# Performance work log

Hardware: AMD Instinct MI355X
Metric: run time of the kernel (lower is better)

The kernel has to match this reference:

```python
import jax, jax.numpy as jnp
import numpy as np

B, T, H_IMG, HID, ACT = 128, 100, 72, 512, 2


def _conv(x, w, b, stride, pad):
    y = jax.lax.conv_general_dilated(
        x, w, (stride, stride), [(pad, pad), (pad, pad)],
        dimension_numbers=('NCHW', 'OIHW', 'NCHW'))
    return y + b[None, :, None, None]


def _encode(images, cw1, cb1, cw2, cb2, cw3, cb3, fw1, fb1, fw2, fb2, fw3, fb3):
    relu = jax.nn.relu
    x = relu(_conv(images, cw1, cb1, 3, 2))   # [B,64,24,24]
    x = relu(_conv(x, cw2, cb2, 3, 2))        # [B,64,9,9]
    x = relu(_conv(x, cw3, cb3, 3, 2))        # [B,64,4,4]
    x = x.reshape(x.shape[0], -1)             # [B,1024]
    x = relu(x @ fw1.T + fb1)
    x = relu(x @ fw2.T + fb2)
    return x @ fw3.T + fb3                    # [B,512]


def _gru(actions, h0, w_ih, w_hh, b_ih, b_hh):
    # precompute input projections for all steps: [T,B,3H]
    gi = jnp.einsum('btd,gd->tbg', actions, w_ih) + b_ih

    def step(h, gi_t):
        gh = h @ w_hh.T + b_hh
        i_r, i_i, i_n = jnp.split(gi_t, 3, axis=-1)
        h_r, h_i, h_n = jnp.split(gh, 3, axis=-1)
        r = jax.nn.sigmoid(i_r + h_r)
        z = jax.nn.sigmoid(i_i + h_i)
        n = jnp.tanh(i_n + r * h_n)
        hy = n + z * (h - n)
        return hy, hy

    hT, outs = jax.lax.scan(step, h0, gi)
    return jnp.transpose(outs, (1, 0, 2)), hT  # batch_first output


def setup_inputs() -> dict:
    key = jax.random.key(0)
    ks = jax.random.split(key, 16)
    s = 0.05
    return {
        'images': jax.random.normal(ks[0], (B, 3, H_IMG, H_IMG), jnp.float32),
        'actions': jax.random.normal(ks[1], (B, T, ACT), jnp.float32),
        'cw1': jax.random.normal(ks[2], (64, 3, 5, 5), jnp.float32) * s,
        'cb1': jax.random.normal(ks[3], (64,), jnp.float32) * s,
        'cw2': jax.random.normal(ks[4], (64, 64, 3, 3), jnp.float32) * s,
        'cb2': jax.random.normal(ks[5], (64,), jnp.float32) * s,
        'cw3': jax.random.normal(ks[6], (64, 64, 3, 3), jnp.float32) * s,
        'cb3': jax.random.normal(ks[7], (64,), jnp.float32) * s,
        'fw1': jax.random.normal(ks[8], (1024, 1024), jnp.float32) * 0.02,
        'fb1': jax.random.normal(ks[9], (1024,), jnp.float32) * 0.02,
        'fw2': jax.random.normal(ks[10], (512, 1024), jnp.float32) * 0.02,
        'fb2': jax.random.normal(ks[11], (512,), jnp.float32) * 0.02,
        'fw3': jax.random.normal(ks[12], (512, 512), jnp.float32) * 0.02,
        'fb3': jax.random.normal(ks[13], (512,), jnp.float32) * 0.02,
        'w_ih': jax.random.normal(ks[14], (3 * HID, ACT), jnp.float32) * 0.05,
        'w_hh': jax.random.normal(ks[15], (3 * HID, HID), jnp.float32) * 0.04,
        'b_ih': jnp.zeros((3 * HID,), jnp.float32),
        'b_hh': jnp.zeros((3 * HID,), jnp.float32),
    }


def reference(images, actions, cw1, cb1, cw2, cb2, cw3, cb3,
              fw1, fb1, fw2, fb2, fw3, fb3, w_ih, w_hh, b_ih, b_hh):
    # Encode the start image to a 512-d representation (BigBasicConv),
    # then integrate the action sequence with the hand-rolled GRU,
    # initial hidden state = start representation.
    h0 = _encode(images, cw1, cb1, cw2, cb2, cw3, cb3,
                 fw1, fb1, fw2, fb2, fw3, fb3)
    output, hT = _gru(actions, h0, w_ih, w_hh, b_ih, b_hh)
    return output, hT
```

## Files before the change

kernel.cpp:

```cpp
#include <hip/hip_runtime.h>
#include <cstdint>

#define BB   128
#define TT   100
#define HID  512

typedef __attribute__((ext_vector_type(4))) float f32x4;
typedef __attribute__((ext_vector_type(2))) float f32x2;
typedef __attribute__((ext_vector_type(8))) short short8;
typedef __attribute__((ext_vector_type(4))) short short4_t;

__device__ __forceinline__ short f2bf(float x) {
  unsigned u = __float_as_uint(x);
  unsigned r = (u + 0x7fffu + ((u >> 16) & 1u)) >> 16;
  return (short)r;
}
__device__ __forceinline__ float bf2f(short s) {
  return __uint_as_float(((unsigned)(unsigned short)s) << 16);
}

__global__ __launch_bounds__(256) void wsplit_k(const float* __restrict__ w,
                                                unsigned short* __restrict__ hi,
                                                unsigned short* __restrict__ lo,
                                                int nq) {
  int i = blockIdx.x * 256 + threadIdx.x;
  const int stride = gridDim.x * 256;
  for (; i < nq; i += stride) {
    f32x4 v = *(const f32x4*)(w + 4 * (long)i);
    short4_t h, l;
    #pragma unroll
    for (int c = 0; c < 4; c++) {
      short hh = f2bf(v[c]); h[c] = hh; l[c] = f2bf(v[c] - bf2f(hh));
    }
    *(short4_t*)(hi + 4 * (long)i) = h;
    *(short4_t*)(lo + 4 * (long)i) = l;
  }
}


__global__ __launch_bounds__(192) void conv1_k(const float* __restrict__ in,
                                               const float* __restrict__ w,
                                               const float* __restrict__ bias,
                                               float* __restrict__ out) {
  const int b = blockIdx.x / 24, oy = blockIdx.x % 24;
  __shared__ __attribute__((aligned(16))) float in_s[3][5][76];
  __shared__ __attribute__((aligned(16))) float ws[64][76];
  const int tid = threadIdx.x;
  for (int i = tid; i < 3 * 5 * 76; i += 192) {
    int ic = i / 380, rem = i % 380, r = rem / 76, p = rem % 76;
    int iy = oy * 3 + r - 2, ix = p - 2;
    in_s[ic][r][p] = (iy >= 0 && iy < 72 && ix >= 0 && ix < 72)
                       ? in[((long)(b * 3 + ic) * 72 + iy) * 72 + ix] : 0.f;
  }
  for (int i = tid; i < 64 * 75; i += 192) ws[i / 75][i % 75] = w[i];
  __syncthreads();

  const int ox2 = tid % 12;
  const int og = tid / 12;
  float strip[15][8];
  #pragma unroll
  for (int ic = 0; ic < 3; ic++)
    #pragma unroll
    for (int ky = 0; ky < 5; ky++) {
      const float* bp = &in_s[ic][ky][6 * ox2];
      #pragma unroll
      for (int h = 0; h < 4; h++) {
        f32x2 u = *(const f32x2*)(bp + 2 * h);
        strip[ic * 5 + ky][2 * h] = u[0];
        strip[ic * 5 + ky][2 * h + 1] = u[1];
      }
    }

  #pragma unroll
  for (int j = 0; j < 4; j++) {
    const int oc = og + 16 * j;
    float s0 = bias[oc], s1 = bias[oc];
    const float* wrow = ws[oc];
    #pragma unroll
    for (int k4 = 0; k4 < 18; k4++) {
      f32x4 wq = *(const f32x4*)(wrow + 4 * k4);
      #pragma unroll
      for (int q = 0; q < 4; q++) {
        const int k = 4 * k4 + q, i5 = k / 5, kx = k % 5;
        s0 += strip[i5][kx] * wq[q];
        s1 += strip[i5][kx + 3] * wq[q];
      }
    }
    s0 += strip[14][2] * wrow[72]; s1 += strip[14][5] * wrow[72];
    s0 += strip[14][3] * wrow[73]; s1 += strip[14][6] * wrow[73];
    s0 += strip[14][4] * wrow[74]; s1 += strip[14][7] * wrow[74];
    long o = ((long)(b * 64 + oc) * 24 + oy) * 24 + 2 * ox2;
    out[o] = fmaxf(s0, 0.f);
    out[o + 1] = fmaxf(s1, 0.f);
  }
}

template <int IC, int IH, int IW, int OC, int OH, int OW>
__global__ void convs3(const float* __restrict__ in, const float* __restrict__ w,
                       const float* __restrict__ bias, float* __restrict__ out) {
  const int b = blockIdx.x / OH, oy = blockIdx.x % OH;
  constexpr int PW = 3 * OW;
  constexpr int NT = (OC / 2) * OW;
  __shared__ __attribute__((aligned(16))) float in_s[8][3][PW];
  __shared__ __attribute__((aligned(16))) float w_s[OC][100];
  const int tid = threadIdx.x;
  const int oc = tid / OW, ox = tid % OW;
  float s0 = bias[oc], s1 = bias[oc + OC / 2];
  for (int cc = 0; cc < IC; cc += 8) {
    __syncthreads();
    for (int i = tid; i < 8 * 3 * PW; i += NT) {
      int ic = i / (3 * PW), r = (i / PW) % 3, p = i % PW;
      int iy = oy * 3 - 2 + r, ix = p - 2;
      in_s[ic][r][p] = (iy >= 0 && iy < IH && ix >= 0 && ix < IW)
                         ? in[((long)(b * IC + cc + ic) * IH + iy) * IW + ix] : 0.f;
    }
    for (int i = tid; i < OC * 8 * 9; i += NT) {
      int o = i / 72, r = i % 72;
      w_s[o][(r / 9) * 12 + (r % 9)] = w[(long)(o * IC + cc + r / 9) * 9 + r % 9];
    }
    __syncthreads();
    #pragma unroll
    for (int ic = 0; ic < 8; ic++) {
      const float* wr0 = &w_s[oc][ic * 12];
      const float* wr1 = &w_s[oc + OC / 2][ic * 12];
      f32x4 wa = *(const f32x4*)wr0, wb = *(const f32x4*)(wr0 + 4);
      f32x4 va = *(const f32x4*)wr1, vb = *(const f32x4*)(wr1 + 4);
      float wA[9] = {wa[0], wa[1], wa[2], wa[3], wb[0], wb[1], wb[2], wb[3], wr0[8]};
      float wB[9] = {va[0], va[1], va[2], va[3], vb[0], vb[1], vb[2], vb[3], wr1[8]};
      #pragma unroll
      for (int ky = 0; ky < 3; ky++)
        #pragma unroll
        for (int kx = 0; kx < 3; kx++) {
          float iv = in_s[ic][ky][ox * 3 + kx];
          s0 += iv * wA[ky * 3 + kx];
          s1 += iv * wB[ky * 3 + kx];
        }
    }
  }
  out[((long)(b * OC + oc) * OH + oy) * OW + ox] = fmaxf(s0, 0.f);
  out[((long)(b * OC + oc + OC / 2) * OH + oy) * OW + ox] = fmaxf(s1, 0.f);
}

template <int K, int N, bool RELU>
__global__ __launch_bounds__(128) void fc_mfma(const float* __restrict__ A,
                                               const unsigned short* __restrict__ wh,
                                               const unsigned short* __restrict__ wl,
                                               const float* __restrict__ bias,
                                               float* __restrict__ C) {
  const int nb = N / 32;
  const int rb = (blockIdx.x / nb) * 16, cb = (blockIdx.x % nb) * 32;
  __shared__ __attribute__((aligned(16))) short A_hi[16][K + 8];
  __shared__ __attribute__((aligned(16))) short A_lo[16][K + 8];
  const int tid = threadIdx.x;
  const int wv = tid >> 6, lane = tid & 63, n16 = lane & 15, quad = lane >> 4;

  for (int i = tid; i < 16 * (K / 4); i += 128) {
    int row = i / (K / 4), q = i % (K / 4);
    f32x4 v = *(const f32x4*)(A + (long)(rb + row) * K + 4 * q);
    short4_t sh, sl;
    #pragma unroll
    for (int c = 0; c < 4; c++) {
      short hh = f2bf(v[c]); sh[c] = hh; sl[c] = f2bf(v[c] - bf2f(hh));
    }
    *(short4_t*)&A_hi[row][4 * q] = sh;
    *(short4_t*)&A_lo[row][4 * q] = sl;
  }
  __syncthreads();

  const int col = cb + wv * 16 + n16;
  f32x4 a0 = {0.f, 0.f, 0.f, 0.f}, a1 = a0, a2 = a0;
  constexpr int NP = K / 512;
  #pragma unroll 1
  for (int p = 0; p < NP; p++) {
    short8 fh[16], fl[16];
    const unsigned short* wb0 = wh + (long)col * K + p * 512 + quad * 8;
    const unsigned short* wb1 = wl + (long)col * K + p * 512 + quad * 8;
    #pragma unroll
    for (int ks = 0; ks < 16; ks++) {
      fh[ks] = *(const short8*)(wb0 + ks * 32);
      fl[ks] = *(const short8*)(wb1 + ks * 32);
    }
    #pragma unroll
    for (int ks = 0; ks < 16; ks++) {
      short8 ah = *(const short8*)&A_hi[n16][p * 512 + ks * 32 + quad * 8];
      short8 al = *(const short8*)&A_lo[n16][p * 512 + ks * 32 + quad * 8];
      a0 = __builtin_amdgcn_mfma_f32_16x16x32_bf16(ah, fh[ks], a0, 0, 0, 0);
      a1 = __builtin_amdgcn_mfma_f32_16x16x32_bf16(al, fh[ks], a1, 0, 0, 0);
      a2 = __builtin_amdgcn_mfma_f32_16x16x32_bf16(ah, fl[ks], a2, 0, 0, 0);
    }
  }
  const float bv = bias[col];
  #pragma unroll
  for (int r = 0; r < 4; r++) {
    float v = a0[r] + a1[r] + a2[r] + bv;
    if (RELU) v = fmaxf(v, 0.f);
    C[(long)(rb + quad * 4 + r) * N + col] = v;
  }
}

__global__ __launch_bounds__(192, 1) void gru_k(
    const float* __restrict__ actions, const float* __restrict__ w_ih,
    const float* __restrict__ w_hh, const float* __restrict__ b_ih,
    const float* __restrict__ b_hh, const float* __restrict__ h0,
    float* __restrict__ out, float* __restrict__ hT, unsigned* __restrict__ bar) {
  const int bg = blockIdx.x >> 5;
  const int hg = blockIdx.x & 31;
  const int tid = threadIdx.x;
  const int wv = tid >> 6;
  const int lane = tid & 63;
  const int n16 = lane & 15;
  const int quad = lane >> 4;

  __shared__ short h_hi[16][520];
  __shared__ short h_lo[16][520];
  __shared__ float act_s[16][2 * TT];
  __shared__ float gh_s[3][16][17];
  __shared__ float bih_s[48], bhh_s[48], wih0_s[48], wih1_s[48];

  short8 whi[16], wlo[16];
  {
    const int grow = wv * HID + hg * 16 + n16;
    const float* wr = w_hh + (long)grow * HID + quad * 8;
    #pragma unroll
    for (int ks = 0; ks < 16; ks++) {
      f32x4 v0 = *(const f32x4*)(wr + ks * 32);
      f32x4 v1 = *(const f32x4*)(wr + ks * 32 + 4);
      short8 hi, lo;
      #pragma unroll
      for (int j = 0; j < 4; j++) {
        short h1 = f2bf(v0[j]); hi[j] = h1;     lo[j] = f2bf(v0[j] - bf2f(h1));
        short h2 = f2bf(v1[j]); hi[j + 4] = h2; lo[j + 4] = f2bf(v1[j] - bf2f(h2));
      }
      whi[ks] = hi; wlo[ks] = lo;
    }
  }
  for (int i = tid; i < 48; i += 192) {
    int row = (i >> 4) * HID + hg * 16 + (i & 15);
    bih_s[i] = b_ih[row];
    bhh_s[i] = b_hh[row];
    wih0_s[i] = w_ih[row * 2];
    wih1_s[i] = w_ih[row * 2 + 1];
  }
  for (int i = tid; i < 16 * 2 * TT; i += 192) {
    int m = i / (2 * TT), r = i % (2 * TT);
    act_s[m][r] = actions[(long)(bg * 16 + m) * (2 * TT) + r];
  }
  for (int i = tid; i < 2048; i += 192) {
    int m = i >> 7, k4 = (i & 127) << 2;
    f32x4 v = *(const f32x4*)(h0 + (long)(bg * 16 + m) * HID + k4);
    short4_t sh, sl;
    #pragma unroll
    for (int c2 = 0; c2 < 4; c2++) {
      short hh = f2bf(v[c2]); sh[c2] = hh; sl[c2] = f2bf(v[c2] - bf2f(hh));
    }
    *(short4_t*)&h_hi[m][k4] = sh;
    *(short4_t*)&h_lo[m][k4] = sl;
  }
  __syncthreads();

  unsigned* my_bar = bar + bg * 32;

  #pragma unroll 1
  for (int t = 0; t < TT; t++) {
    f32x4 a0 = {0.f, 0.f, 0.f, 0.f}, a1 = a0, a2 = a0;
    #pragma unroll
    for (int ks = 0; ks < 16; ks++) {
      short8 ah = *(const short8*)&h_hi[n16][ks * 32 + quad * 8];
      short8 al = *(const short8*)&h_lo[n16][ks * 32 + quad * 8];
      a0 = __builtin_amdgcn_mfma_f32_16x16x32_bf16(ah, whi[ks], a0, 0, 0, 0);
      a1 = __builtin_amdgcn_mfma_f32_16x16x32_bf16(al, whi[ks], a1, 0, 0, 0);
      a2 = __builtin_amdgcn_mfma_f32_16x16x32_bf16(ah, wlo[ks], a2, 0, 0, 0);
    }
    #pragma unroll
    for (int r = 0; r < 4; r++)
      gh_s[wv][quad * 4 + r][n16] = a0[r] + a1[r] + a2[r];
    __syncthreads();

    if (tid < 128) {
      const int m = tid >> 3;
      const int n0 = (tid & 7) << 1;
      const float x0 = act_s[m][2 * t], x1 = act_s[m][2 * t + 1];
      float hy[2];
      #pragma unroll
      for (int q = 0; q < 2; q++) {
        int n = n0 + q;
        float hr = gh_s[0][m][n] + bhh_s[n];
        float hz = gh_s[1][m][n] + bhh_s[16 + n];
        float hn = gh_s[2][m][n] + bhh_s[32 + n];
        float ir = x0 * wih0_s[n]      + x1 * wih1_s[n]      + bih_s[n];
        float iz = x0 * wih0_s[16 + n] + x1 * wih1_s[16 + n] + bih_s[16 + n];
        float in_ = x0 * wih0_s[32 + n] + x1 * wih1_s[32 + n] + bih_s[32 + n];
        float rg = 1.f / (1.f + __expf(-(ir + hr)));
        float zg = 1.f / (1.f + __expf(-(iz + hz)));
        float nx = in_ + rg * hn;
        float ng = 1.f - 2.f / (__expf(2.f * nx) + 1.f);
        float hprev = bf2f(h_hi[m][hg * 16 + n]) + bf2f(h_lo[m][hg * 16 + n]);
        hy[q] = ng + zg * (hprev - ng);
      }
      unsigned long long pack = (unsigned long long)__float_as_uint(hy[0]) |
                                ((unsigned long long)__float_as_uint(hy[1]) << 32);
      __hip_atomic_store(
          (unsigned long long*)&out[((long)(bg * 16 + m) * TT + t) * HID + hg * 16 + n0],
          pack, __ATOMIC_RELAXED, __HIP_MEMORY_SCOPE_AGENT);
      if (t == TT - 1)
        *(unsigned long long*)&hT[(long)(bg * 16 + m) * HID + hg * 16 + n0] = pack;
    }
    __syncthreads();

    if (t < TT - 1) {
      if (tid == 0) {
        const unsigned target = 32u * (unsigned)(t + 1);
        unsigned prev = __hip_atomic_fetch_add(my_bar, 1u, __ATOMIC_RELAXED,
                                               __HIP_MEMORY_SCOPE_AGENT);
        if (prev + 1u < target) {
          while (__hip_atomic_load(my_bar, __ATOMIC_RELAXED,
                                   __HIP_MEMORY_SCOPE_AGENT) < target)
            __builtin_amdgcn_s_sleep(1);
        }
      }
      __syncthreads();
      unsigned long long vbuf[22];
      #pragma unroll
      for (int u = 0; u < 21; u++) {
        int i = tid + u * 192;
        int m = i >> 8, j = (i & 255) << 1;
        vbuf[u] = __hip_atomic_load(
            (const unsigned long long*)(out + ((long)(bg * 16 + m) * TT + t) * HID + j),
            __ATOMIC_RELAXED, __HIP_MEMORY_SCOPE_AGENT);
      }
      if (tid < 64) {
        int i = 4032 + tid;
        int m = i >> 8, j = (i & 255) << 1;
        vbuf[21] = __hip_atomic_load(
            (const unsigned long long*)(out + ((long)(bg * 16 + m) * TT + t) * HID + j),
            __ATOMIC_RELAXED, __HIP_MEMORY_SCOPE_AGENT);
      }
      #pragma unroll
      for (int u = 0; u < 21; u++) {
        int i = tid + u * 192;
        int m = i >> 8, j = (i & 255) << 1;
        unsigned long long v = vbuf[u];
        float f0 = __uint_as_float((unsigned)v);
        float f1 = __uint_as_float((unsigned)(v >> 32));
        short s0 = f2bf(f0);
        h_hi[m][j] = s0; h_lo[m][j] = f2bf(f0 - bf2f(s0));
        short s1 = f2bf(f1);
        h_hi[m][j + 1] = s1; h_lo[m][j + 1] = f2bf(f1 - bf2f(s1));
      }
      if (tid < 64) {
        int i = 4032 + tid;
        int m = i >> 8, j = (i & 255) << 1;
        unsigned long long v = vbuf[21];
        float f0 = __uint_as_float((unsigned)v);
        float f1 = __uint_as_float((unsigned)(v >> 32));
        short s0 = f2bf(f0);
        h_hi[m][j] = s0; h_lo[m][j] = f2bf(f0 - bf2f(s0));
        short s1 = f2bf(f1);
        h_hi[m][j + 1] = s1; h_lo[m][j + 1] = f2bf(f1 - bf2f(s1));
      }
      __syncthreads();
    }
  }
}

extern "C" void kernel_launch(void* const* d_in, const int* in_sizes, int n_in,
                              void* d_out, int out_size, void* d_ws, size_t ws_size,
                              hipStream_t stream) {
  const float* images  = (const float*)d_in[0];
  const float* actions = (const float*)d_in[1];
  const float* cw1 = (const float*)d_in[2];
  const float* cb1 = (const float*)d_in[3];
  const float* cw2 = (const float*)d_in[4];
  const float* cb2 = (const float*)d_in[5];
  const float* cw3 = (const float*)d_in[6];
  const float* cb3 = (const float*)d_in[7];
  const float* fw1 = (const float*)d_in[8];
  const float* fb1 = (const float*)d_in[9];
  const float* fw2 = (const float*)d_in[10];
  const float* fb2 = (const float*)d_in[11];
  const float* fw3 = (const float*)d_in[12];
  const float* fb3 = (const float*)d_in[13];
  const float* w_ih = (const float*)d_in[14];
  const float* w_hh = (const float*)d_in[15];
  const float* b_ih = (const float*)d_in[16];
  const float* b_hh = (const float*)d_in[17];

  char* ws = (char*)d_ws;
  unsigned* bar = (unsigned*)ws;
  float* a1 = (float*)(ws + 1024);
  float* a2 = a1 + (long)128 * 64 * 576;
  float* a3 = a2 + (long)128 * 64 * 81;
  float* f1 = a3 + (long)128 * 1024;
  float* f2 = f1 + (long)128 * 1024;
  float* h0 = f2 + (long)128 * 512;
  unsigned short* wfh1 = (unsigned short*)(h0 + 65536);
  unsigned short* wfl1 = wfh1 + (long)1048576;
  unsigned short* wfh2 = wfl1 + (long)1048576;
  unsigned short* wfl2 = wfh2 + (long)524288;
  unsigned short* wfh3 = wfl2 + (long)524288;
  unsigned short* wfl3 = wfh3 + (long)262144;

  float* out = (float*)d_out;
  float* hT  = out + (long)BB * TT * HID;

  hipMemsetAsync(bar, 0, 1024, stream);
  wsplit_k<<<256, 256, 0, stream>>>(fw1, wfh1, wfl1, 262144);
  wsplit_k<<<128, 256, 0, stream>>>(fw2, wfh2, wfl2, 131072);
  wsplit_k<<<64, 256, 0, stream>>>(fw3, wfh3, wfl3, 65536);
  conv1_k<<<128 * 24, 192, 0, stream>>>(images, cw1, cb1, a1);
  convs3<64, 24, 24, 64, 9, 9><<<128 * 9, 288, 0, stream>>>(a1, cw2, cb2, a2);
  convs3<64, 9, 9, 64, 4, 4><<<128 * 4, 128, 0, stream>>>(a2, cw3, cb3, a3);
  fc_mfma<1024, 1024, true><<<256, 128, 0, stream>>>(a3, wfh1, wfl1, fb1, f1);
  fc_mfma<1024, 512, true><<<128, 128, 0, stream>>>(f1, wfh2, wfl2, fb2, f2);
  fc_mfma<512, 512, false><<<128, 128, 0, stream>>>(f2, wfh3, wfl3, fb3, h0);
  gru_k<<<256, 192, 0, stream>>>(actions, w_ih, w_hh, b_ih, b_hh, h0, out, hT, bar);
}
```

Before: 645.1 us.

## Fuse conv2, conv3, FC layers and GRU into one persistent kernel

Merges conv2, conv3, the three FC layers and the GRU into a single persistent 256-block kernel, with grid-wide atomic barriers between phases in place of separate launches. The three weight-split kernels also become one launch, and the GRU carries its previous hidden state in registers. The goal is to remove launch overhead and inter-kernel gaps. In exchange, the conv phases are re-tiled onto a fixed grid of 256 blocks with 192 threads, which may lower per-phase efficiency, and the spin barriers depend on all 256 blocks being co-resident.

```diff
diff --git a/kernel.cpp b/kernel.cpp
--- a/kernel.cpp
+++ b/kernel.cpp
@@ -9,6 +9,7 @@
 typedef __attribute__((ext_vector_type(2))) float f32x2;
 typedef __attribute__((ext_vector_type(8))) short short8;
 typedef __attribute__((ext_vector_type(4))) short short4_t;
+typedef unsigned long long ull;
 
 __device__ __forceinline__ short f2bf(float x) {
   unsigned u = __float_as_uint(x);
@@ -18,25 +19,45 @@
 __device__ __forceinline__ float bf2f(short s) {
   return __uint_as_float(((unsigned)(unsigned short)s) << 16);
 }
-
-__global__ __launch_bounds__(256) void wsplit_k(const float* __restrict__ w,
-                                                unsigned short* __restrict__ hi,
-                                                unsigned short* __restrict__ lo,
-                                                int nq) {
+__device__ __forceinline__ ull aload8(const void* p) {
+  return __hip_atomic_load((const ull*)p, __ATOMIC_RELAXED, __HIP_MEMORY_SCOPE_AGENT);
+}
+__device__ __forceinline__ void astore8(void* p, ull v) {
+  __hip_atomic_store((ull*)p, v, __ATOMIC_RELAXED, __HIP_MEMORY_SCOPE_AGENT);
+}
+__device__ __forceinline__ float aloadf(const float* p) {
+  unsigned v = __hip_atomic_load((const unsigned*)p, __ATOMIC_RELAXED,
+                                 __HIP_MEMORY_SCOPE_AGENT);
+  return __uint_as_float(v);
+}
+__device__ __forceinline__ void astoref(float* p, float x) {
+  __hip_atomic_store((unsigned*)p, __float_as_uint(x), __ATOMIC_RELAXED,
+                     __HIP_MEMORY_SCOPE_AGENT);
+}
+
+__global__ __launch_bounds__(256) void wsplit_all(
+    const float* __restrict__ w1, const float* __restrict__ w2,
+    const float* __restrict__ w3, unsigned short* __restrict__ h1,
+    unsigned short* __restrict__ l1, unsigned short* __restrict__ h2,
+    unsigned short* __restrict__ l2, unsigned short* __restrict__ h3,
+    unsigned short* __restrict__ l3) {
   int i = blockIdx.x * 256 + threadIdx.x;
   const int stride = gridDim.x * 256;
-  for (; i < nq; i += stride) {
-    f32x4 v = *(const f32x4*)(w + 4 * (long)i);
+  for (; i < 458752; i += stride) {
+    const float* src; unsigned short *ph, *pl; int j;
+    if (i < 262144)      { src = w1; ph = h1; pl = l1; j = i; }
+    else if (i < 393216) { src = w2; ph = h2; pl = l2; j = i - 262144; }
+    else                 { src = w3; ph = h3; pl = l3; j = i - 393216; }
+    f32x4 v = *(const f32x4*)(src + 4 * (long)j);
     short4_t h, l;
     #pragma unroll
     for (int c = 0; c < 4; c++) {
       short hh = f2bf(v[c]); h[c] = hh; l[c] = f2bf(v[c] - bf2f(hh));
     }
-    *(short4_t*)(hi + 4 * (long)i) = h;
-    *(short4_t*)(lo + 4 * (long)i) = l;
-  }
-}
-
+    *(short4_t*)(ph + 4 * (long)j) = h;
+    *(short4_t*)(pl + 4 * (long)j) = l;
+  }
+}
 
 __global__ __launch_bounds__(192) void conv1_k(const float* __restrict__ in,
                                                const float* __restrict__ w,
@@ -95,270 +116,402 @@
   }
 }
 
-template <int IC, int IH, int IW, int OC, int OH, int OW>
-__global__ void convs3(const float* __restrict__ in, const float* __restrict__ w,
-                       const float* __restrict__ bias, float* __restrict__ out) {
-  const int b = blockIdx.x / OH, oy = blockIdx.x % OH;
-  constexpr int PW = 3 * OW;
-  constexpr int NT = (OC / 2) * OW;
-  __shared__ __attribute__((aligned(16))) float in_s[8][3][PW];
-  __shared__ __attribute__((aligned(16))) float w_s[OC][100];
-  const int tid = threadIdx.x;
-  const int oc = tid / OW, ox = tid % OW;
-  float s0 = bias[oc], s1 = bias[oc + OC / 2];
-  for (int cc = 0; cc < IC; cc += 8) {
-    __syncthreads();
-    for (int i = tid; i < 8 * 3 * PW; i += NT) {
-      int ic = i / (3 * PW), r = (i / PW) % 3, p = i % PW;
-      int iy = oy * 3 - 2 + r, ix = p - 2;
-      in_s[ic][r][p] = (iy >= 0 && iy < IH && ix >= 0 && ix < IW)
-                         ? in[((long)(b * IC + cc + ic) * IH + iy) * IW + ix] : 0.f;
-    }
-    for (int i = tid; i < OC * 8 * 9; i += NT) {
-      int o = i / 72, r = i % 72;
-      w_s[o][(r / 9) * 12 + (r % 9)] = w[(long)(o * IC + cc + r / 9) * 9 + r % 9];
-    }
-    __syncthreads();
-    #pragma unroll
-    for (int ic = 0; ic < 8; ic++) {
-      const float* wr0 = &w_s[oc][ic * 12];
-      const float* wr1 = &w_s[oc + OC / 2][ic * 12];
-      f32x4 wa = *(const f32x4*)wr0, wb = *(const f32x4*)(wr0 + 4);
-      f32x4 va = *(const f32x4*)wr1, vb = *(const f32x4*)(wr1 + 4);
-      float wA[9] = {wa[0], wa[1], wa[2], wa[3], wb[0], wb[1], wb[2], wb[3], wr0[8]};
-      float wB[9] = {va[0], va[1], va[2], va[3], vb[0], vb[1], vb[2], vb[3], wr1[8]};
-      #pragma unroll
-      for (int ky = 0; ky < 3; ky++)
-        #pragma unroll
-        for (int kx = 0; kx < 3; kx++) {
-          float iv = in_s[ic][ky][ox * 3 + kx];
-          s0 += iv * wA[ky * 3 + kx];
-          s1 += iv * wB[ky * 3 + kx];
-        }
-    }
-  }
-  out[((long)(b * OC + oc) * OH + oy) * OW + ox] = fmaxf(s0, 0.f);
-  out[((long)(b * OC + oc + OC / 2) * OH + oy) * OW + ox] = fmaxf(s1, 0.f);
+
+__device__ __forceinline__ void gbarrier(unsigned* c) {
+  __syncthreads();
+  if (threadIdx.x == 0) {
+    __hip_atomic_fetch_add(c, 1u, __ATOMIC_RELAXED, __HIP_MEMORY_SCOPE_AGENT);
+    while (__hip_atomic_load(c, __ATOMIC_RELAXED, __HIP_MEMORY_SCOPE_AGENT) < 256u)
+      __builtin_amdgcn_s_sleep(2);
+  }
+  __syncthreads();
 }
 
 template <int K, int N, bool RELU>
-__global__ __launch_bounds__(128) void fc_mfma(const float* __restrict__ A,
-                                               const unsigned short* __restrict__ wh,
-                                               const unsigned short* __restrict__ wl,
-                                               const float* __restrict__ bias,
-                                               float* __restrict__ C) {
+__device__ __forceinline__ void fc_phase(int bid, int tid, const float* A,
+    const unsigned short* wh, const unsigned short* wl, const float* bias,
+    float* C, char* smem) {
   const int nb = N / 32;
-  const int rb = (blockIdx.x / nb) * 16, cb = (blockIdx.x % nb) * 32;
-  __shared__ __attribute__((aligned(16))) short A_hi[16][K + 8];
-  __shared__ __attribute__((aligned(16))) short A_lo[16][K + 8];
-  const int tid = threadIdx.x;
+  if (bid >= (BB / 16) * nb) return;
+  short (*A_hi)[520] = (short(*)[520])smem;
+  short (*A_lo)[520] = (short(*)[520])(smem + 16 * 520 * 2);
+  const int rb = (bid / nb) * 16, cb = (bid % nb) * 32;
   const int wv = tid >> 6, lane = tid & 63, n16 = lane & 15, quad = lane >> 4;
-
-  for (int i = tid; i < 16 * (K / 4); i += 128) {
-    int row = i / (K / 4), q = i % (K / 4);
-    f32x4 v = *(const f32x4*)(A + (long)(rb + row) * K + 4 * q);
-    short4_t sh, sl;
-    #pragma unroll
-    for (int c = 0; c < 4; c++) {
-      short hh = f2bf(v[c]); sh[c] = hh; sl[c] = f2bf(v[c] - bf2f(hh));
-    }
-    *(short4_t*)&A_hi[row][4 * q] = sh;
-    *(short4_t*)&A_lo[row][4 * q] = sl;
-  }
-  __syncthreads();
-
   const int col = cb + wv * 16 + n16;
   f32x4 a0 = {0.f, 0.f, 0.f, 0.f}, a1 = a0, a2 = a0;
-  constexpr int NP = K / 512;
   #pragma unroll 1
-  for (int p = 0; p < NP; p++) {
-    short8 fh[16], fl[16];
-    const unsigned short* wb0 = wh + (long)col * K + p * 512 + quad * 8;
-    const unsigned short* wb1 = wl + (long)col * K + p * 512 + quad * 8;
+  for (int p = 0; p < K / 512; p++) {
+    if (p) __syncthreads();
+    for (int i = tid; i < 2048; i += 192) {
+      int row = i >> 7, q = i & 127;
+      const float* src = A + (long)(rb + row) * K + p * 512 + 4 * q;
+      union { ull u[2]; float f[4]; } v;
+      v.u[0] = aload8(src); v.u[1] = aload8(src + 2);
+      short4_t sh, sl;
+      #pragma unroll
+      for (int c = 0; c < 4; c++) {
+        short hh = f2bf(v.f[c]); sh[c] = hh; sl[c] = f2bf(v.f[c] - bf2f(hh));
+      }
+      *(short4_t*)&A_hi[row][4 * q] = sh;
+      *(short4_t*)&A_lo[row][4 * q] = sl;
+    }
+    __syncthreads();
+    if (tid < 128) {
+      const unsigned short* wb0 = wh + (long)col * K + p * 512 + quad * 8;
+      const unsigned short* wb1 = wl + (long)col * K + p * 512 + quad * 8;
+      short8 fh[16], fl[16];
+      #pragma unroll
+      for (int ks = 0; ks < 16; ks++) {
+        fh[ks] = *(const short8*)(wb0 + ks * 32);
+        fl[ks] = *(const short8*)(wb1 + ks * 32);
+      }
+      #pragma unroll
+      for (int ks = 0; ks < 16; ks++) {
+        short8 ah = *(const short8*)&A_hi[n16][ks * 32 + quad * 8];
+        short8 al = *(const short8*)&A_lo[n16][ks * 32 + quad * 8];
+        a0 = __builtin_amdgcn_mfma_f32_16x16x32_bf16(ah, fh[ks], a0, 0, 0, 0);
+        a1 = __builtin_amdgcn_mfma_f32_16x16x32_bf16(al, fh[ks], a1, 0, 0, 0);
+        a2 = __builtin_amdgcn_mfma_f32_16x16x32_bf16(ah, fl[ks], a2, 0, 0, 0);
+      }
+    }
+  }
+  if (tid < 128) {
+    const float bv = bias[col];
     #pragma unroll
-    for (int ks = 0; ks < 16; ks++) {
-      fh[ks] = *(const short8*)(wb0 + ks * 32);
-      fl[ks] = *(const short8*)(wb1 + ks * 32);
-    }
-    #pragma unroll
-    for (int ks = 0; ks < 16; ks++) {
-      short8 ah = *(const short8*)&A_hi[n16][p * 512 + ks * 32 + quad * 8];
-      short8 al = *(const short8*)&A_lo[n16][p * 512 + ks * 32 + quad * 8];
-      a0 = __builtin_amdgcn_mfma_f32_16x16x32_bf16(ah, fh[ks], a0, 0, 0, 0);
-      a1 = __builtin_amdgcn_mfma_f32_16x16x32_bf16(al, fh[ks], a1, 0, 0, 0);
-      a2 = __builtin_amdgcn_mfma_f32_16x16x32_bf16(ah, fl[ks], a2, 0, 0, 0);
-    }
-  }
-  const float bv = bias[col];
-  #pragma unroll
-  for (int r = 0; r < 4; r++) {
-    float v = a0[r] + a1[r] + a2[r] + bv;
-    if (RELU) v = fmaxf(v, 0.f);
-    C[(long)(rb + quad * 4 + r) * N + col] = v;
-  }
-}
-
-__global__ __launch_bounds__(192, 1) void gru_k(
+    for (int r = 0; r < 4; r++) {
+      float v = a0[r] + a1[r] + a2[r] + bv;
+      if (RELU) v = fmaxf(v, 0.f);
+      astoref(&C[(long)(rb + quad * 4 + r) * N + col], v);
+    }
+  }
+}
+
+__global__ __launch_bounds__(192, 1) void mega_k(
+    const float* __restrict__ a1, const float* __restrict__ cw2,
+    const float* __restrict__ cb2, const float* __restrict__ cw3,
+    const float* __restrict__ cb3,
+    const unsigned short* __restrict__ wfh1, const unsigned short* __restrict__ wfl1,
+    const float* __restrict__ fb1,
+    const unsigned short* __restrict__ wfh2, const unsigned short* __restrict__ wfl2,
+    const float* __restrict__ fb2,
+    const unsigned short* __restrict__ wfh3, const unsigned short* __restrict__ wfl3,
+    const float* __restrict__ fb3,
     const float* __restrict__ actions, const float* __restrict__ w_ih,
     const float* __restrict__ w_hh, const float* __restrict__ b_ih,
-    const float* __restrict__ b_hh, const float* __restrict__ h0,
-    float* __restrict__ out, float* __restrict__ hT, unsigned* __restrict__ bar) {
-  const int bg = blockIdx.x >> 5;
-  const int hg = blockIdx.x & 31;
+    const float* __restrict__ b_hh,
+    float* __restrict__ a2, float* __restrict__ a3, float* __restrict__ f1,
+    float* __restrict__ f2, float* __restrict__ h0,
+    float* __restrict__ out, float* __restrict__ hT,
+    unsigned* __restrict__ bar, unsigned* __restrict__ gctr) {
+  __shared__ __attribute__((aligned(16))) char smem[50176];
+  const int bid = blockIdx.x;
   const int tid = threadIdx.x;
-  const int wv = tid >> 6;
-  const int lane = tid & 63;
-  const int n16 = lane & 15;
-  const int quad = lane >> 4;
-
-  __shared__ short h_hi[16][520];
-  __shared__ short h_lo[16][520];
-  __shared__ float act_s[16][2 * TT];
-  __shared__ float gh_s[3][16][17];
-  __shared__ float bih_s[48], bhh_s[48], wih0_s[48], wih1_s[48];
-
-  short8 whi[16], wlo[16];
+
   {
-    const int grow = wv * HID + hg * 16 + n16;
-    const float* wr = w_hh + (long)grow * HID + quad * 8;
-    #pragma unroll
-    for (int ks = 0; ks < 16; ks++) {
-      f32x4 v0 = *(const f32x4*)(wr + ks * 32);
-      f32x4 v1 = *(const f32x4*)(wr + ks * 32 + 4);
-      short8 hi, lo;
-      #pragma unroll
-      for (int j = 0; j < 4; j++) {
-        short h1 = f2bf(v0[j]); hi[j] = h1;     lo[j] = f2bf(v0[j] - bf2f(h1));
-        short h2 = f2bf(v1[j]); hi[j + 4] = h2; lo[j + 4] = f2bf(v1[j] - bf2f(h2));
-      }
-      whi[ks] = hi; wlo[ks] = lo;
-    }
-  }
-  for (int i = tid; i < 48; i += 192) {
-    int row = (i >> 4) * HID + hg * 16 + (i & 15);
-    bih_s[i] = b_ih[row];
-    bhh_s[i] = b_hh[row];
-    wih0_s[i] = w_ih[row * 2];
-    wih1_s[i] = w_ih[row * 2 + 1];
-  }
-  for (int i = tid; i < 16 * 2 * TT; i += 192) {
-    int m = i / (2 * TT), r = i % (2 * TT);
-    act_s[m][r] = actions[(long)(bg * 16 + m) * (2 * TT) + r];
-  }
-  for (int i = tid; i < 2048; i += 192) {
-    int m = i >> 7, k4 = (i & 127) << 2;
-    f32x4 v = *(const f32x4*)(h0 + (long)(bg * 16 + m) * HID + k4);
-    short4_t sh, sl;
-    #pragma unroll
-    for (int c2 = 0; c2 < 4; c2++) {
-      short hh = f2bf(v[c2]); sh[c2] = hh; sl[c2] = f2bf(v[c2] - bf2f(hh));
-    }
-    *(short4_t*)&h_hi[m][k4] = sh;
-    *(short4_t*)&h_lo[m][k4] = sl;
-  }
-  __syncthreads();
-
-  unsigned* my_bar = bar + bg * 32;
-
-  #pragma unroll 1
-  for (int t = 0; t < TT; t++) {
-    f32x4 a0 = {0.f, 0.f, 0.f, 0.f}, a1 = a0, a2 = a0;
-    #pragma unroll
-    for (int ks = 0; ks < 16; ks++) {
-      short8 ah = *(const short8*)&h_hi[n16][ks * 32 + quad * 8];
-      short8 al = *(const short8*)&h_lo[n16][ks * 32 + quad * 8];
-      a0 = __builtin_amdgcn_mfma_f32_16x16x32_bf16(ah, whi[ks], a0, 0, 0, 0);
-      a1 = __builtin_amdgcn_mfma_f32_16x16x32_bf16(al, whi[ks], a1, 0, 0, 0);
-      a2 = __builtin_amdgcn_mfma_f32_16x16x32_bf16(ah, wlo[ks], a2, 0, 0, 0);
-    }
-    #pragma unroll
-    for (int r = 0; r < 4; r++)
-      gh_s[wv][quad * 4 + r][n16] = a0[r] + a1[r] + a2[r];
+    float (*w_s)[100] = (float(*)[100])smem;
+    float* in2 = (float*)(smem + 25600);
+    const int q = tid / 9, ox = tid % 9;
+    float acc[5][4];
+    if (tid < 144) {
+      #pragma unroll
+      for (int t5 = 0; t5 < 5; t5++)
+        #pragma unroll
+        for (int j = 0; j < 4; j++) acc[t5][j] = cb2[q + 16 * j];
+    }
+    for (int cc = 0; cc < 64; cc += 8) {
+      __syncthreads();
+      for (int i = tid; i < 4608; i += 192) {
+        int o = i / 72, r = i % 72;
+        w_s[o][(r / 9) * 12 + (r % 9)] = cw2[(long)(o * 64 + cc + r / 9) * 9 + r % 9];
+      }
+      for (int i = tid; i < 3240; i += 192) {
+        int t5 = i / 648, r = i % 648;
+        int tile = bid + t5 * 256;
+        if (tile < 1152) {
+          int b = tile / 9, oy = tile % 9;
+          int ic = r / 81, rr = (r / 27) % 3, p = r % 27;
+          int iy = oy * 3 - 2 + rr, ix = p - 2;
+          in2[t5 * 648 + ic * 81 + rr * 27 + p] =
+              (iy >= 0 && iy < 24 && ix >= 0 && ix < 24)
+                ? a1[((long)(b * 64 + cc + ic) * 24 + iy) * 24 + ix] : 0.f;
+        }
+      }
+      __syncthreads();
+      if (tid < 144) {
+        #pragma unroll
+        for (int ic = 0; ic < 8; ic++) {
+          float wq[4][9];
+          #pragma unroll
+          for (int j = 0; j < 4; j++) {
+            const float* wr = &w_s[q + 16 * j][ic * 12];
+            f32x4 wa = *(const f32x4*)wr, wb = *(const f32x4*)(wr + 4);
+            wq[j][0] = wa[0]; wq[j][1] = wa[1]; wq[j][2] = wa[2]; wq[j][3] = wa[3];
+            wq[j][4] = wb[0]; wq[j][5] = wb[1]; wq[j][6] = wb[2]; wq[j][7] = wb[3];
+            wq[j][8] = wr[8];
+          }
+          #pragma unroll
+          for (int t5 = 0; t5 < 5; t5++) {
+            if (bid + t5 * 256 < 1152) {
+              #pragma unroll
+              for (int ky = 0; ky < 3; ky++)
+                #pragma unroll
+                for (int kx = 0; kx < 3; kx++) {
+                  float iv = in2[t5 * 648 + ic * 81 + ky * 27 + ox * 3 + kx];
+                  #pragma unroll
+                  for (int j = 0; j < 4; j++) acc[t5][j] += iv * wq[j][ky * 3 + kx];
+                }
+            }
+          }
+        }
+      }
+    }
+    if (tid < 144) {
+      #pragma unroll
+      for (int t5 = 0; t5 < 5; t5++) {
+        int tile = bid + t5 * 256;
+        if (tile < 1152) {
+          int b = tile / 9, oy = tile % 9;
+          #pragma unroll
+          for (int j = 0; j < 4; j++)
+            astoref(&a2[((long)(b * 64 + q + 16 * j) * 9 + oy) * 9 + ox],
+                    fmaxf(acc[t5][j], 0.f));
+        }
+      }
+    }
+  }
+  gbarrier(gctr + 0);
+
+  {
+    float (*w_s)[100] = (float(*)[100])smem;
+    float* in3 = (float*)(smem + 25600);
+    const int oc = tid >> 2, ox = tid & 3;
+    float acc[2][2];
+    if (tid < 128) {
+      acc[0][0] = acc[1][0] = cb3[oc];
+      acc[0][1] = acc[1][1] = cb3[oc + 32];
+    }
+    for (int cc = 0; cc < 64; cc += 8) {
+      __syncthreads();
+      for (int i = tid; i < 4608; i += 192) {
+        int o = i / 72, r = i % 72;
+        w_s[o][(r / 9) * 12 + (r % 9)] = cw3[(long)(o * 64 + cc + r / 9) * 9 + r % 9];
+      }
+      for (int i = tid; i < 576; i += 192) {
+        int t2 = i / 288, r = i % 288;
+        int tile = bid + t2 * 256;
+        int b = tile / 4, oy = tile % 4;
+        int ic = r / 36, rr = (r / 12) % 3, p = r % 12;
+        int iy = oy * 3 - 2 + rr, ix = p - 2;
+        in3[t2 * 288 + ic * 36 + rr * 12 + p] =
+            (iy >= 0 && iy < 9 && ix >= 0 && ix < 9)
+              ? aloadf(&a2[((long)(b * 64 + cc + ic) * 9 + iy) * 9 + ix]) : 0.f;
+      }
+      __syncthreads();
+      if (tid < 128) {
+        #pragma unroll
+        for (int ic = 0; ic < 8; ic++) {
+          const float* wr0 = &w_s[oc][ic * 12];
+          const float* wr1 = &w_s[oc + 32][ic * 12];
+          f32x4 wa = *(const f32x4*)wr0, wb = *(const f32x4*)(wr0 + 4);
+          f32x4 va = *(const f32x4*)wr1, vb = *(const f32x4*)(wr1 + 4);
+          float wA[9] = {wa[0], wa[1], wa[2], wa[3], wb[0], wb[1], wb[2], wb[3], wr0[8]};
+          float wB[9] = {va[0], va[1], va[2], va[3], vb[0], vb[1], vb[2], vb[3], wr1[8]};
+          #pragma unroll
+          for (int t2 = 0; t2 < 2; t2++)
+            #pragma unroll
+            for (int ky = 0; ky < 3; ky++)
+              #pragma unroll
+              for (int kx = 0; kx < 3; kx++) {
+                float iv = in3[t2 * 288 + ic * 36 + ky * 12 + ox * 3 + kx];
+                acc[t2][0] += iv * wA[ky * 3 + kx];
+                acc[t2][1] += iv * wB[ky * 3 + kx];
+              }
+        }
+      }
+    }
+    if (tid < 128) {
+      #pragma unroll
+      for (int t2 = 0; t2 < 2; t2++) {
+        int tile = bid + t2 * 256;
+        int b = tile / 4, oy = tile % 4;
+        astoref(&a3[((long)(b * 64 + oc) * 4 + oy) * 4 + ox], fmaxf(acc[t2][0], 0.f));
+        astoref(&a3[((long)(b * 64 + oc + 32) * 4 + oy) * 4 + ox], fmaxf(acc[t2][1], 0.f));
+      }
+    }
+  }
+  gbarrier(gctr + 1);
+
+  fc_phase<1024, 1024, true>(bid, tid, a3, wfh1, wfl1, fb1, f1, smem);
+  gbarrier(gctr + 2);
+  fc_phase<1024, 512, true>(bid, tid, f1, wfh2, wfl2, fb2, f2, smem);
+  gbarrier(gctr + 3);
+  fc_phase<512, 512, false>(bid, tid, f2, wfh3, wfl3, fb3, h0, smem);
+  gbarrier(gctr + 4);
+
+  {
+    short (*h_hi)[520] = (short(*)[520])smem;
+    short (*h_lo)[520] = (short(*)[520])(smem + 16640);
+    float (*act_s)[200] = (float(*)[200])(smem + 33280);
+    float (*gh_s)[16][17] = (float(*)[16][17])(smem + 46080);
+    float* bih_s = (float*)(smem + 49344);
+    float* bhh_s = bih_s + 48;
+    float* wih0_s = bhh_s + 48;
+    float* wih1_s = wih0_s + 48;
+
+    const int bg = bid >> 5;
+    const int hg = bid & 31;
+    const int wv = tid >> 6;
+    const int lane = tid & 63;
+    const int n16 = lane & 15;
+    const int quad = lane >> 4;
+
+    short8 whi[16], wlo[16];
+    {
+      const int grow = wv * HID + hg * 16 + n16;
+      const float* wr = w_hh + (long)grow * HID + quad * 8;
+      #pragma unroll
+      for (int ks = 0; ks < 16; ks++) {
+        f32x4 v0 = *(const f32x4*)(wr + ks * 32);
+        f32x4 v1 = *(const f32x4*)(wr + ks * 32 + 4);
+        short8 hi, lo;
+        #pragma unroll
+        for (int j = 0; j < 4; j++) {
+          short h1 = f2bf(v0[j]); hi[j] = h1;     lo[j] = f2bf(v0[j] - bf2f(h1));
+          short h2 = f2bf(v1[j]); hi[j + 4] = h2; lo[j + 4] = f2bf(v1[j] - bf2f(h2));
+        }
+        whi[ks] = hi; wlo[ks] = lo;
+      }
+    }
+    for (int i = tid; i < 48; i += 192) {
+      int row = (i >> 4) * HID + hg * 16 + (i & 15);
+      bih_s[i] = b_ih[row];
+      bhh_s[i] = b_hh[row];
+      wih0_s[i] = w_ih[row * 2];
+      wih1_s[i] = w_ih[row * 2 + 1];
+    }
+    for (int i = tid; i < 16 * 2 * TT; i += 192) {
+      int m = i / (2 * TT), r = i % (2 * TT);
+      act_s[m][r] = actions[(long)(bg * 16 + m) * (2 * TT) + r];
+    }
+    for (int i = tid; i < 2048; i += 192) {
+      int m = i >> 7, k4 = (i & 127) << 2;
+      const float* src = h0 + (long)(bg * 16 + m) * HID + k4;
+      union { ull u[2]; float f[4]; } v;
+      v.u[0] = aload8(src); v.u[1] = aload8(src + 2);
+      short4_t sh, sl;
+      #pragma unroll
+      for (int c2 = 0; c2 < 4; c2++) {
+        short hh = f2bf(v.f[c2]); sh[c2] = hh; sl[c2] = f2bf(v.f[c2] - bf2f(hh));
+      }
+      *(short4_t*)&h_hi[m][k4] = sh;
+      *(short4_t*)&h_lo[m][k4] = sl;
+    }
+    float hp0 = 0.f, hp1 = 0.f;
+    if (tid < 128) {
+      const int m = tid >> 3, n0 = (tid & 7) << 1;
+      union { ull u; float f[2]; } v;
+      v.u = aload8(h0 + (long)(bg * 16 + m) * HID + hg * 16 + n0);
+      hp0 = v.f[0]; hp1 = v.f[1];
+    }
     __syncthreads();
 
-    if (tid < 128) {
-      const int m = tid >> 3;
-      const int n0 = (tid & 7) << 1;
-      const float x0 = act_s[m][2 * t], x1 = act_s[m][2 * t + 1];
-      float hy[2];
-      #pragma unroll
-      for (int q = 0; q < 2; q++) {
-        int n = n0 + q;
-        float hr = gh_s[0][m][n] + bhh_s[n];
-        float hz = gh_s[1][m][n] + bhh_s[16 + n];
-        float hn = gh_s[2][m][n] + bhh_s[32 + n];
-        float ir = x0 * wih0_s[n]      + x1 * wih1_s[n]      + bih_s[n];
-        float iz = x0 * wih0_s[16 + n] + x1 * wih1_s[16 + n] + bih_s[16 + n];
-        float in_ = x0 * wih0_s[32 + n] + x1 * wih1_s[32 + n] + bih_s[32 + n];
-        float rg = 1.f / (1.f + __expf(-(ir + hr)));
-        float zg = 1.f / (1.f + __expf(-(iz + hz)));
-        float nx = in_ + rg * hn;
-        float ng = 1.f - 2.f / (__expf(2.f * nx) + 1.f);
-        float hprev = bf2f(h_hi[m][hg * 16 + n]) + bf2f(h_lo[m][hg * 16 + n]);
-        hy[q] = ng + zg * (hprev - ng);
-      }
-      unsigned long long pack = (unsigned long long)__float_as_uint(hy[0]) |
-                                ((unsigned long long)__float_as_uint(hy[1]) << 32);
-      __hip_atomic_store(
-          (unsigned long long*)&out[((long)(bg * 16 + m) * TT + t) * HID + hg * 16 + n0],
-          pack, __ATOMIC_RELAXED, __HIP_MEMORY_SCOPE_AGENT);
-      if (t == TT - 1)
-        *(unsigned long long*)&hT[(long)(bg * 16 + m) * HID + hg * 16 + n0] = pack;
-    }
-    __syncthreads();
-
-    if (t < TT - 1) {
-      if (tid == 0) {
-        const unsigned target = 32u * (unsigned)(t + 1);
-        unsigned prev = __hip_atomic_fetch_add(my_bar, 1u, __ATOMIC_RELAXED,
-                                               __HIP_MEMORY_SCOPE_AGENT);
-        if (prev + 1u < target) {
-          while (__hip_atomic_load(my_bar, __ATOMIC_RELAXED,
-                                   __HIP_MEMORY_SCOPE_AGENT) < target)
-            __builtin_amdgcn_s_sleep(1);
-        }
-      }
+    unsigned* my_bar = bar + bg * 32;
+
+    #pragma unroll 1
+    for (int t = 0; t < TT; t++) {
+      f32x4 a0 = {0.f, 0.f, 0.f, 0.f}, a1 = a0, a2 = a0;
+      #pragma unroll
+      for (int ks = 0; ks < 16; ks++) {
+        short8 ah = *(const short8*)&h_hi[n16][ks * 32 + quad * 8];
+        short8 al = *(const short8*)&h_lo[n16][ks * 32 + quad * 8];
+        a0 = __builtin_amdgcn_mfma_f32_16x16x32_bf16(ah, whi[ks], a0, 0, 0, 0);
+        a1 = __builtin_amdgcn_mfma_f32_16x16x32_bf16(al, whi[ks], a1, 0, 0, 0);
+        a2 = __builtin_amdgcn_mfma_f32_16x16x32_bf16(ah, wlo[ks], a2, 0, 0, 0);
+      }
+      #pragma unroll
+      for (int r = 0; r < 4; r++)
+        gh_s[wv][quad * 4 + r][n16] = a0[r] + a1[r] + a2[r];
       __syncthreads();
-      unsigned long long vbuf[22];
-      #pragma unroll
-      for (int u = 0; u < 21; u++) {
-        int i = tid + u * 192;
-        int m = i >> 8, j = (i & 255) << 1;
-        vbuf[u] = __hip_atomic_load(
-            (const unsigned long long*)(out + ((long)(bg * 16 + m) * TT + t) * HID + j),
-            __ATOMIC_RELAXED, __HIP_MEMORY_SCOPE_AGENT);
-      }
-      if (tid < 64) {
-        int i = 4032 + tid;
-        int m = i >> 8, j = (i & 255) << 1;
-        vbuf[21] = __hip_atomic_load(
-            (const unsigned long long*)(out + ((long)(bg * 16 + m) * TT + t) * HID + j),
-            __ATOMIC_RELAXED, __HIP_MEMORY_SCOPE_AGENT);
-      }
-      #pragma unroll
-      for (int u = 0; u < 21; u++) {
-        int i = tid + u * 192;
-        int m = i >> 8, j = (i & 255) << 1;
-        unsigned long long v = vbuf[u];
-        float f0 = __uint_as_float((unsigned)v);
-        float f1 = __uint_as_float((unsigned)(v >> 32));
-        short s0 = f2bf(f0);
-        h_hi[m][j] = s0; h_lo[m][j] = f2bf(f0 - bf2f(s0));
-        short s1 = f2bf(f1);
-        h_hi[m][j + 1] = s1; h_lo[m][j + 1] = f2bf(f1 - bf2f(s1));
-      }
-      if (tid < 64) {
-        int i = 4032 + tid;
-        int m = i >> 8, j = (i & 255) << 1;
-        unsigned long long v = vbuf[21];
-        float f0 = __uint_as_float((unsigned)v);
-        float f1 = __uint_as_float((unsigned)(v >> 32));
-        short s0 = f2bf(f0);
-        h_hi[m][j] = s0; h_lo[m][j] = f2bf(f0 - bf2f(s0));
-        short s1 = f2bf(f1);
-        h_hi[m][j + 1] = s1; h_lo[m][j + 1] = f2bf(f1 - bf2f(s1));
+
+      if (tid < 128) {
+        const int m = tid >> 3;
+        const int n0 = (tid & 7) << 1;
+        const float x0 = act_s[m][2 * t], x1 = act_s[m][2 * t + 1];
+        float hy[2];
+        #pragma unroll
+        for (int q = 0; q < 2; q++) {
+          int n = n0 + q;
+          float hr = gh_s[0][m][n] + bhh_s[n];
+          float hz = gh_s[1][m][n] + bhh_s[16 + n];
+          float hn = gh_s[2][m][n] + bhh_s[32 + n];
+          float ir = x0 * wih0_s[n]      + x1 * wih1_s[n]      + bih_s[n];
+          float iz = x0 * wih0_s[16 + n] + x1 * wih1_s[16 + n] + bih_s[16 + n];
+          float in_ = x0 * wih0_s[32 + n] + x1 * wih1_s[32 + n] + bih_s[32 + n];
+          float rg = 1.f / (1.f + __expf(-(ir + hr)));
+          float zg = 1.f / (1.f + __expf(-(iz + hz)));
+          float nx = in_ + rg * hn;
+          float ng = 1.f - 2.f / (__expf(2.f * nx) + 1.f);
+          float hprev = q ? hp1 : hp0;
+          hy[q] = ng + zg * (hprev - ng);
+        }
+        hp0 = hy[0]; hp1 = hy[1];
+        ull pack = (ull)__float_as_uint(hy[0]) |
+                   ((ull)__float_as_uint(hy[1]) << 32);
+        astore8(&out[((long)(bg * 16 + m) * TT + t) * HID + hg * 16 + n0], pack);
+        if (t == TT - 1)
+          *(ull*)&hT[(long)(bg * 16 + m) * HID + hg * 16 + n0] = pack;
       }
       __syncthreads();
+
+      if (t < TT - 1) {
+        if (tid == 0) {
+          const unsigned target = 32u * (unsigned)(t + 1);
+          unsigned prev = __hip_atomic_fetch_add(my_bar, 1u, __ATOMIC_RELAXED,
+                                                 __HIP_MEMORY_SCOPE_AGENT);
+          if (prev + 1u < target) {
+            while (__hip_atomic_load(my_bar, __ATOMIC_RELAXED,
+                                     __HIP_MEMORY_SCOPE_AGENT) < target)
+              __builtin_amdgcn_s_sleep(1);
+          }
+        }
+        __syncthreads();
+        ull vbuf[22];
+        #pragma unroll
+        for (int u = 0; u < 21; u++) {
+          int i = tid + u * 192;
+          int m = i >> 8, j = (i & 255) << 1;
+          vbuf[u] = aload8(out + ((long)(bg * 16 + m) * TT + t) * HID + j);
+        }
+        if (tid < 64) {
+          int i = 4032 + tid;
+          int m = i >> 8, j = (i & 255) << 1;
+          vbuf[21] = aload8(out + ((long)(bg * 16 + m) * TT + t) * HID + j);
+        }
+        #pragma unroll
+        for (int u = 0; u < 21; u++) {
+          int i = tid + u * 192;
+          int m = i >> 8, j = (i & 255) << 1;
+          ull v = vbuf[u];
+          float f0 = __uint_as_float((unsigned)v);
+          float f1 = __uint_as_float((unsigned)(v >> 32));
+          short s0 = f2bf(f0);
+          h_hi[m][j] = s0; h_lo[m][j] = f2bf(f0 - bf2f(s0));
+          short s1 = f2bf(f1);
+          h_hi[m][j + 1] = s1; h_lo[m][j + 1] = f2bf(f1 - bf2f(s1));
+        }
+        if (tid < 64) {
+          int i = 4032 + tid;
+          int m = i >> 8, j = (i & 255) << 1;
+          ull v = vbuf[21];
+          float f0 = __uint_as_float((unsigned)v);
+          float f1 = __uint_as_float((unsigned)(v >> 32));
+          short s0 = f2bf(f0);
+          h_hi[m][j] = s0; h_lo[m][j] = f2bf(f0 - bf2f(s0));
+          short s1 = f2bf(f1);
+          h_hi[m][j + 1] = s1; h_lo[m][j + 1] = f2bf(f1 - bf2f(s1));
+        }
+        __syncthreads();
+      }
     }
   }
 }
@@ -387,7 +540,8 @@
 
   char* ws = (char*)d_ws;
   unsigned* bar = (unsigned*)ws;
-  float* a1 = (float*)(ws + 1024);
+  unsigned* gctr = (unsigned*)(ws + 1024);
+  float* a1 = (float*)(ws + 2048);
   float* a2 = a1 + (long)128 * 64 * 576;
   float* a3 = a2 + (long)128 * 64 * 81;
   float* f1 = a3 + (long)128 * 1024;
@@ -403,15 +557,13 @@
   float* out = (float*)d_out;
   float* hT  = out + (long)BB * TT * HID;
 
-  hipMemsetAsync(bar, 0, 1024, stream);
-  wsplit_k<<<256, 256, 0, stream>>>(fw1, wfh1, wfl1, 262144);
-  wsplit_k<<<128, 256, 0, stream>>>(fw2, wfh2, wfl2, 131072);
-  wsplit_k<<<64, 256, 0, stream>>>(fw3, wfh3, wfl3, 65536);
+  hipMemsetAsync(ws, 0, 2048, stream);
+  wsplit_all<<<448, 256, 0, stream>>>(fw1, fw2, fw3, wfh1, wfl1, wfh2, wfl2,
+                                      wfh3, wfl3);
   conv1_k<<<128 * 24, 192, 0, stream>>>(images, cw1, cb1, a1);
-  convs3<64, 24, 24, 64, 9, 9><<<128 * 9, 288, 0, stream>>>(a1, cw2, cb2, a2);
-  convs3<64, 9, 9, 64, 4, 4><<<128 * 4, 128, 0, stream>>>(a2, cw3, cb3, a3);
-  fc_mfma<1024, 1024, true><<<256, 128, 0, stream>>>(a3, wfh1, wfl1, fb1, f1);
-  fc_mfma<1024, 512, true><<<128, 128, 0, stream>>>(f1, wfh2, wfl2, fb2, f2);
-  fc_mfma<512, 512, false><<<128, 128, 0, stream>>>(f2, wfh3, wfl3, fb3, h0);
-  gru_k<<<256, 192, 0, stream>>>(actions, w_ih, w_hh, b_ih, b_hh, h0, out, hT, bar);
-}
+  mega_k<<<256, 192, 0, stream>>>(a1, cw2, cb2, cw3, cb3,
+                                  wfh1, wfl1, fb1, wfh2, wfl2, fb2,
+                                  wfh3, wfl3, fb3,
+                                  actions, w_ih, w_hh, b_ih, b_hh,
+                                  a2, a3, f1, f2, h0, out, hT, bar, gctr);
+}
```

After: 697.3 us. 1.08x slower.
